# Kernel optimization log

Hardware: AMD Instinct MI355X
Metric: run time of the kernel (lower is better)

The kernel has to match this reference:

```python
import jax, jax.numpy as jnp
import numpy as np

N = 100000      # nodes
E = 1600000     # edges (avg degree 16)
F_IN = 128      # num_features
H = 128         # hidden_channels
OUT = 64        # out_channels


def _glorot(key, shape):
    lim = float(np.sqrt(6.0 / (shape[0] + shape[1])))
    return jax.random.uniform(key, shape, jnp.float32, -lim, lim)


def setup_inputs() -> dict:
    key = jax.random.key(0)
    ks = jax.random.split(key, 5)
    x = jax.random.normal(ks[0], (N, F_IN), jnp.float32)
    edge_index = jax.random.randint(ks[1], (2, E), 0, N, dtype=jnp.int64)
    W1 = _glorot(ks[2], (F_IN, H)); b1 = jnp.zeros((H,), jnp.float32)
    W2 = _glorot(ks[3], (H, H));    b2 = jnp.zeros((H,), jnp.float32)
    W3 = _glorot(ks[4], (H, OUT));  b3 = jnp.zeros((OUT,), jnp.float32)
    return {"x": x, "edge_index": edge_index,
            "W1": W1, "b1": b1, "W2": W2, "b2": b2, "W3": W3, "b3": b3}


def _gcn_conv(h, src, dst, norm, W, b, n):
    # PyG GCNConv: linear transform, then sym-normalized scatter aggregation, then bias
    h = h @ W                                   # [N, d_out]
    msg = h[src] * norm[:, None]                # gather + scale, [E+N, d_out]
    agg = jax.ops.segment_sum(msg, dst, num_segments=n)
    return agg + b


def reference(x, edge_index, W1, b1, W2, b2, W3, b3):
    n = x.shape[0]
    # add self-loops (GCNConv default add_self_loops=True)
    loop = jnp.arange(n, dtype=edge_index.dtype)
    src = jnp.concatenate([edge_index[0], loop])
    dst = jnp.concatenate([edge_index[1], loop])
    # symmetric normalization deg^-1/2[src] * deg^-1/2[dst]
    deg = jax.ops.segment_sum(jnp.ones_like(dst, x.dtype), dst, num_segments=n)
    dinv = jnp.where(deg > 0, jax.lax.rsqrt(deg), 0.0)
    norm = dinv[src] * dinv[dst]

    h = jax.nn.relu(_gcn_conv(x, src, dst, norm, W1, b1, n))  # dropout p=0 -> no-op
    h = jax.nn.relu(_gcn_conv(h, src, dst, norm, W2, b2, n))
    h = _gcn_conv(h, src, dst, norm, W3, b3, n)
    return jax.nn.log_softmax(h, axis=1)
```

## Files before the change

### kernel.cpp

```cpp
#include <hip/hip_runtime.h>
#include <stdint.h>
#include <math.h>

#define FIN 128

typedef __attribute__((ext_vector_type(8))) short short8v;
typedef __attribute__((ext_vector_type(4))) float float4v;
typedef __attribute__((ext_vector_type(2))) float float2v;

__device__ __forceinline__ uint32_t f2_to_bf2(float x, float y) {
    uint32_t r;
    asm("v_cvt_pk_bf16_f32 %0, %1, %2" : "=v"(r) : "v"(x), "v"(y));
    return r;
}
__device__ __forceinline__ unsigned short f_to_bf(float x) {
    union { float f; uint32_t i; } a;
    a.f = x;
    uint32_t u = a.i + 0x7FFF + ((a.i >> 16) & 1);
    return (unsigned short)(u >> 16);
}
__device__ __forceinline__ void acc16_fp8_pk(float2v* acc2, uint4 v) {
    uint32_t us[4] = {v.x, v.y, v.z, v.w};
#pragma unroll
    for (int q = 0; q < 4; ++q) {
        acc2[q * 2 + 0] += __builtin_amdgcn_cvt_pk_f32_fp8(us[q], false);
        acc2[q * 2 + 1] += __builtin_amdgcn_cvt_pk_f32_fp8(us[q], true);
    }
}

template <int CTRL>
__device__ __forceinline__ float dppmov(float x) {
    int i = __builtin_bit_cast(int, x);
    int r = __builtin_amdgcn_update_dpp(i, i, CTRL, 0xF, 0xF, false);
    return __builtin_bit_cast(float, r);
}
__device__ __forceinline__ float swz16f(float x) {
    int r = __builtin_amdgcn_ds_swizzle(__builtin_bit_cast(int, x), 0x401F);
    return __builtin_bit_cast(float, r);
}

__device__ __forceinline__ int edge_at(const void* ei, long long idx, int is32) {
    return is32 ? ((const int*)ei)[idx] : (int)((const long long*)ei)[idx];
}

#define SP_CHUNK 4096
__global__ __launch_bounds__(256) void splitA_kernel(const void* __restrict__ ei,
                                                     int* __restrict__ gCnt,
                                                     uint32_t* __restrict__ buf1,
                                                     int E, int capS) {
    __shared__ int hist[16];
    __shared__ int gbase[16];
    __shared__ int lflag;
    int t = threadIdx.x;
    if (t < 16) hist[t] = 0;
    if (t == 0) lflag = 0;
    long long base = (long long)blockIdx.x * SP_CHUNK;
    __syncthreads();
    {
        long long e = base + t;
        if (e < E && ((const int*)ei)[2 * e + 1] != 0) atomicOr(&lflag, 1);
    }
    __syncthreads();
    int is32 = lflag;
    uint32_t lrec[16], rec[16];
#pragma unroll
    for (int j = 0; j < 16; ++j) {
        long long e = base + t + j * 256;
        if (e < E) {
            int s = edge_at(ei, e, is32);
            int d = edge_at(ei, (long long)E + e, is32);
            int b = d >> 13;
            int lofs = atomicAdd(&hist[b], 1);
            lrec[j] = ((uint32_t)lofs << 4) | (uint32_t)b;
            rec[j] = ((uint32_t)s << 13) | (uint32_t)(d & 8191);
        } else
            lrec[j] = 0xFFFFFFFFu;
    }
    __syncthreads();
    if (t < 16) gbase[t] = atomicAdd(&gCnt[t], hist[t]);
    __syncthreads();
#pragma unroll
    for (int j = 0; j < 16; ++j) {
        if (lrec[j] != 0xFFFFFFFFu) {
            int b = lrec[j] & 15;
            int pos = gbase[b] + (int)(lrec[j] >> 4);
            if (pos < capS) buf1[(size_t)b * capS + pos] = rec[j];
        }
    }
}

__global__ __launch_bounds__(256) void splitB_kernel(const int* __restrict__ gCnt,
                                                     const uint32_t* __restrict__ buf1,
                                                     int* __restrict__ cnt2,
                                                     uint32_t* __restrict__ buf2,
                                                     int capS, int cap2, int NB) {
    __shared__ int hist[128];
    __shared__ int gbase[128];
    int t = threadIdx.x;
    int s = blockIdx.y;
    if (t < 128) hist[t] = 0;
    __syncthreads();
    int m = gCnt[s];
    if (m > capS) m = capS;
    long long base = (long long)blockIdx.x * SP_CHUNK;
    uint32_t lrec[16], r32[16];
#pragma unroll
    for (int j = 0; j < 16; ++j) {
        long long i = base + t + j * 256;
        if (i < m) {
            uint32_t r = buf1[(size_t)s * capS + i];
            int d13 = (int)(r & 8191u);
            int sub = d13 >> 6;
            int lofs = atomicAdd(&hist[sub], 1);
            lrec[j] = ((uint32_t)lofs << 7) | (uint32_t)sub;
            r32[j] = ((r >> 13) << 6) | (uint32_t)(d13 & 63);
        } else
            lrec[j] = 0xFFFFFFFFu;
    }
    __syncthreads();
    if (t < 128) {
        int g = s * 128 + t;
        gbase[t] = (g < NB) ? atomicAdd(&cnt2[g], hist[t]) : 0;
    }
    __syncthreads();
#pragma unroll
    for (int j = 0; j < 16; ++j) {
        if (lrec[j] != 0xFFFFFFFFu) {
            int sub = lrec[j] & 127;
            int pos = gbase[sub] + (int)(lrec[j] >> 7);
            if (pos < cap2) buf2[(size_t)(s * 128 + sub) * cap2 + pos] = r32[j];
        }
    }
}

__global__ __launch_bounds__(256) void binBC_kernel(const int* __restrict__ cnt2,
                                                    const uint32_t* __restrict__ buf2,
                                                    int* __restrict__ cnt,
                                                    float* __restrict__ dinv,
                                                    int* __restrict__ rowstart,
                                                    int* __restrict__ col,
                                                    int n, int cap2) {
    __shared__ int h[64];
    __shared__ int rowst[64];
    __shared__ int cur[64];
    __shared__ int sc[64];
    int bin = blockIdx.x;
    int t = threadIdx.x;
    if (t < 64) {
        h[t] = (bin * 64 + t < n) ? 1 : 0;
        cur[t] = 1;
    }
    __syncthreads();
    int m = cnt2[bin];
    if (m > cap2) m = cap2;
    const uint32_t* buf = buf2 + (size_t)bin * cap2;
    for (int i = t; i < m; i += 256) atomicAdd(&h[buf[i] & 63], 1);
    __syncthreads();
    int c = 0, pc = 0;
    if (t < 64) { c = h[t]; pc = (c + 3) & ~3; sc[t] = pc; }
    __syncthreads();
    for (int off = 1; off < 64; off <<= 1) {
        int v = 0;
        if (t < 64 && t >= off) v = sc[t - off];
        __syncthreads();
        if (t < 64) sc[t] += v;
        __syncthreads();
    }
    if (t < 64) {
        int node = bin * 64 + t;
        int base = bin * cap2;
        int st = base + sc[t] - pc;
        rowst[t] = st;
        if (node < n) {
            cnt[node] = c;
            dinv[node] = rsqrtf((float)c);
            rowstart[node] = st;
            col[st] = node;
            for (int k = c; k < pc; ++k) col[st + k] = n;
        }
    }
    __syncthreads();
    for (int i = t; i < m; i += 256) {
        uint32_t rec = buf[i];
        int d6 = rec & 63;
        int off = atomicAdd(&cur[d6], 1);
        col[rowst[d6] + off] = (int)(rec >> 6);
    }
}

__global__ __launch_bounds__(256) void wconv_all(const float* __restrict__ W1,
                                                 const float* __restrict__ W2,
                                                 const float* __restrict__ W3,
                                                 unsigned short* __restrict__ Wf1,
                                                 unsigned short* __restrict__ Wf2,
                                                 unsigned short* __restrict__ Wf3) {
    int idx = blockIdx.x * 256 + threadIdx.x;
    const float* W;
    unsigned short* Wf;
    int NCOL, base;
    if (idx < 2048)      { W = W1; Wf = Wf1; NCOL = 128; base = idx; }
    else if (idx < 4096) { W = W2; Wf = Wf2; NCOL = 128; base = idx - 2048; }
    else if (idx < 5120) { W = W3; Wf = Wf3; NCOL = 64;  base = idx - 4096; }
    else return;
    int f = base >> 6, l = base & 63;
    int ct = f >> 2, ks = f & 3;
    int nn = ct * 16 + (l & 15);
    int k0 = ks * 32 + (l >> 4) * 8;
    uint32_t pk[4];
#pragma unroll
    for (int j = 0; j < 4; ++j) {
        float a = W[(size_t)(k0 + 2 * j) * NCOL + nn];
        float b = W[(size_t)(k0 + 2 * j + 1) * NCOL + nn];
        pk[j] = f2_to_bf2(a, b);
    }
    uint4 v = make_uint4(pk[0], pk[1], pk[2], pk[3]);
    ((uint4*)Wf)[base] = v;
}

template <int NCOL, int A_FP32, int OUT_FP8>
__global__ __launch_bounds__(256) void gemm_mfma(const void* __restrict__ Av,
                                                 const unsigned short* __restrict__ Wf,
                                                 const float* __restrict__ dinv,
                                                 void* __restrict__ Cv, int n) {
    __shared__ unsigned short lds[NCOL * 128];
    const int t = threadIdx.x;
    if (blockIdx.x == 0 && t < NCOL / 4)
        ((uint32_t*)Cv)[(size_t)n * (NCOL / 4) + t] = 0;
    for (int i = t; i < NCOL * 16; i += 256)
        ((uint4*)lds)[i] = ((const uint4*)Wf)[i];
    __syncthreads();

    const int wave = t >> 6, lane = t & 63;
    const int row0 = blockIdx.x * 64 + wave * 16;
    const int m = lane & 15, quad = lane >> 4;
    int arow = row0 + m;
    if (arow >= n) arow = n - 1;

    short8v a[4];
    if (A_FP32) {
        const float* A = (const float*)Av;
#pragma unroll
        for (int ks = 0; ks < 4; ++ks) {
            float4 lo = *(const float4*)(A + (size_t)arow * 128 + ks * 32 + quad * 8);
            float4 hi = *(const float4*)(A + (size_t)arow * 128 + ks * 32 + quad * 8 + 4);
            union { short8v v; uint32_t u[4]; } pk;
            pk.u[0] = f2_to_bf2(lo.x, lo.y);
            pk.u[1] = f2_to_bf2(lo.z, lo.w);
            pk.u[2] = f2_to_bf2(hi.x, hi.y);
            pk.u[3] = f2_to_bf2(hi.z, hi.w);
            a[ks] = pk.v;
        }
    } else {
        const unsigned short* A = (const unsigned short*)Av;
#pragma unroll
        for (int ks = 0; ks < 4; ++ks)
            a[ks] = *(const short8v*)(A + (size_t)arow * 128 + ks * 32 + quad * 8);
    }

    const int cr0 = row0 + quad * 4;
    float ds[4];
#pragma unroll
    for (int r = 0; r < 4; ++r) {
        int gr = cr0 + r;
        ds[r] = (gr < n) ? dinv[gr] : 0.0f;
    }
#pragma unroll
    for (int ct = 0; ct < NCOL / 16; ++ct) {
        float4v acc = {0.0f, 0.0f, 0.0f, 0.0f};
#pragma unroll
        for (int ks = 0; ks < 4; ++ks) {
            int f = ct * 4 + ks;
            short8v b = *(const short8v*)(lds + ((size_t)(f * 64 + lane)) * 8);
            acc = __builtin_amdgcn_mfma_f32_16x16x32_bf16(a[ks], b, acc, 0, 0, 0);
        }
#pragma unroll
        for (int r = 0; r < 4; ++r) {
            int gr = cr0 + r;
            if (gr < n) {
                float val = acc[r] * ds[r];
                if (OUT_FP8) {
                    int u = __builtin_amdgcn_cvt_pk_fp8_f32(val, val, 0, false);
                    ((unsigned char*)Cv)[(size_t)gr * NCOL + ct * 16 + m] =
                        (unsigned char)(u & 0xFF);
                } else {
                    ((unsigned short*)Cv)[(size_t)gr * NCOL + ct * 16 + m] = f_to_bf(val);
                }
            }
        }
    }
}

__global__ __launch_bounds__(256) void agg_relu_128_fp8(
        const uint32_t* __restrict__ T8, const int* __restrict__ rowstart,
        const int* __restrict__ cnt, const int* __restrict__ col,
        const float* __restrict__ dinv, const float* __restrict__ bias,
        uint32_t* __restrict__ outHb, int n) {
    int wid = blockIdx.x * 4 + (threadIdx.x >> 6);
    int lane = threadIdx.x & 63;
    int slot = lane & 3, j = (lane >> 2) & 7, sel = lane >> 5;
    int nodeA = wid * 2;
    int node = nodeA + sel;
    if (nodeA >= n) return;
    bool valid = node < n;
    int nd = valid ? node : nodeA;
    int start = rowstart[nd];
    int c = cnt[nd];
    int nit = valid ? (((c + 3) & ~3) >> 2) : 0;

    float2v acc2[8];
#pragma unroll
    for (int k = 0; k < 8; ++k) acc2[k] = (float2v){0.0f, 0.0f};
    const uint4* T4 = (const uint4*)T8;
    int bp = start + slot;
    int s0 = col[bp];
    s0 = (0 < nit) ? s0 : n;
    uint4 vN = T4[(size_t)s0 * 8 + j];
    int s1 = col[bp + 4];
    s1 = (1 < nit) ? s1 : n;
    uint4 vM = T4[(size_t)s1 * 8 + j];
    for (int it = 0; it < nit; ++it) {
        int s2 = col[bp + (it + 2) * 4];
        s2 = (it + 2 < nit) ? s2 : n;
        uint4 vP = T4[(size_t)s2 * 8 + j];
        acc16_fp8_pk(acc2, vN);
        vN = vM;
        vM = vP;
    }
    float* acc = (float*)acc2;
#pragma unroll
    for (int k = 0; k < 16; ++k) acc[k] += dppmov<0xB1>(acc[k]);
#pragma unroll
    for (int k = 0; k < 16; ++k) acc[k] += dppmov<0x4E>(acc[k]);
    if (slot == 0 && valid) {
        float di = dinv[node];
        const float4* b4 = (const float4*)bias;
        float r[16];
#pragma unroll
        for (int q = 0; q < 4; ++q) {
            float4 bb = b4[j * 4 + q];
            r[q * 4 + 0] = fmaxf(di * acc[q * 4 + 0] + bb.x, 0.0f);
            r[q * 4 + 1] = fmaxf(di * acc[q * 4 + 1] + bb.y, 0.0f);
            r[q * 4 + 2] = fmaxf(di * acc[q * 4 + 2] + bb.z, 0.0f);
            r[q * 4 + 3] = fmaxf(di * acc[q * 4 + 3] + bb.w, 0.0f);
        }
        uint4 o0, o1;
        o0.x = f2_to_bf2(r[0], r[1]);   o0.y = f2_to_bf2(r[2], r[3]);
        o0.z = f2_to_bf2(r[4], r[5]);   o0.w = f2_to_bf2(r[6], r[7]);
        o1.x = f2_to_bf2(r[8], r[9]);   o1.y = f2_to_bf2(r[10], r[11]);
        o1.z = f2_to_bf2(r[12], r[13]); o1.w = f2_to_bf2(r[14], r[15]);
        *(uint4*)(outHb + (size_t)node * 64 + j * 8) = o0;
        *(uint4*)(outHb + (size_t)node * 64 + j * 8 + 4) = o1;
    }
}

__global__ __launch_bounds__(256) void agg_lsm_64_fp8(
        const uint32_t* __restrict__ T8, const int* __restrict__ rowstart,
        const int* __restrict__ cnt, const int* __restrict__ col,
        const float* __restrict__ dinv, const float* __restrict__ bias,
        float* __restrict__ out, int n) {
    int wid = blockIdx.x * 4 + (threadIdx.x >> 6);
    int lane = threadIdx.x & 63;
    int slot = (lane & 3) + ((lane >> 4) & 1) * 4;
    int j = (lane >> 2) & 3, sel = lane >> 5;
    int nodeA = wid * 2;
    int node = nodeA + sel;
    if (nodeA >= n) return;
    bool valid = node < n;
    int nd = valid ? node : nodeA;
    int start = rowstart[nd];
    int c = cnt[nd];
    int pend = valid ? (start + ((c + 3) & ~3)) : start;
    int nit = valid ? (((c + 3) & ~3) + 7) >> 3 : 0;

    float2v acc2[8];
#pragma unroll
    for (int k = 0; k < 8; ++k) acc2[k] = (float2v){0.0f, 0.0f};
    const uint4* T4 = (const uint4*)T8;
    int bp = start + slot;
    int i0 = bp;
    int s0 = col[i0];
    s0 = (i0 < pend) ? s0 : n;
    uint4 vN = T4[(size_t)s0 * 4 + j];
    int i1 = bp + 8;
    int s1 = col[i1];
    s1 = (i1 < pend) ? s1 : n;
    uint4 vM = T4[(size_t)s1 * 4 + j];
    for (int it = 0; it < nit; ++it) {
        int i2 = bp + (it + 2) * 8;
        int s2 = col[i2];
        s2 = (i2 < pend) ? s2 : n;
        uint4 vP = T4[(size_t)s2 * 4 + j];
        acc16_fp8_pk(acc2, vN);
        vN = vM;
        vM = vP;
    }
    float* acc = (float*)acc2;
#pragma unroll
    for (int k = 0; k < 16; ++k) acc[k] += dppmov<0xB1>(acc[k]);
#pragma unroll
    for (int k = 0; k < 16; ++k) acc[k] += dppmov<0x4E>(acc[k]);
#pragma unroll
    for (int k = 0; k < 16; ++k) acc[k] += swz16f(acc[k]);
    float di = dinv[nd];
    const float4* b4 = (const float4*)bias;
    float r[16];
#pragma unroll
    for (int q = 0; q < 4; ++q) {
        float4 bb = b4[j * 4 + q];
        r[q * 4 + 0] = di * acc[q * 4 + 0] + bb.x;
        r[q * 4 + 1] = di * acc[q * 4 + 1] + bb.y;
        r[q * 4 + 2] = di * acc[q * 4 + 2] + bb.z;
        r[q * 4 + 3] = di * acc[q * 4 + 3] + bb.w;
    }
    float m0 = fmaxf(fmaxf(r[0], r[1]), fmaxf(r[2], r[3]));
    float m1 = fmaxf(fmaxf(r[4], r[5]), fmaxf(r[6], r[7]));
    float m2 = fmaxf(fmaxf(r[8], r[9]), fmaxf(r[10], r[11]));
    float m3 = fmaxf(fmaxf(r[12], r[13]), fmaxf(r[14], r[15]));
    float m = fmaxf(fmaxf(m0, m1), fmaxf(m2, m3));
    m = fmaxf(m, dppmov<0x124>(m));
    m = fmaxf(m, dppmov<0x128>(m));
    float e0 = __expf(r[0] - m) + __expf(r[1] - m) + __expf(r[2] - m) +
               __expf(r[3] - m);
    float e1 = __expf(r[4] - m) + __expf(r[5] - m) + __expf(r[6] - m) +
               __expf(r[7] - m);
    float e2 = __expf(r[8] - m) + __expf(r[9] - m) + __expf(r[10] - m) +
               __expf(r[11] - m);
    float e3 = __expf(r[12] - m) + __expf(r[13] - m) + __expf(r[14] - m) +
               __expf(r[15] - m);
    float ss = (e0 + e1) + (e2 + e3);
    ss += dppmov<0x124>(ss);
    ss += dppmov<0x128>(ss);
    float lg = m + __logf(ss);
    if (slot == 0 && valid) {
#pragma unroll
        for (int q = 0; q < 4; ++q) {
            float4 o = make_float4(r[q * 4 + 0] - lg, r[q * 4 + 1] - lg,
                                   r[q * 4 + 2] - lg, r[q * 4 + 3] - lg);
            *(float4*)(out + (size_t)node * 64 + j * 16 + q * 4) = o;
        }
    }
}

extern "C" void kernel_launch(void* const* d_in, const int* in_sizes, int n_in,
                              void* d_out, int out_size, void* d_ws, size_t ws_size,
                              hipStream_t stream) {
    const float* x  = (const float*)d_in[0];
    const void*  ei = d_in[1];
    const float* W1 = (const float*)d_in[2];
    const float* b1 = (const float*)d_in[3];
    const float* W2 = (const float*)d_in[4];
    const float* b2 = (const float*)d_in[5];
    const float* W3 = (const float*)d_in[6];
    const float* b3 = (const float*)d_in[7];
    float* out = (float*)d_out;

    const int n = in_sizes[0] / FIN;
    const int E = in_sizes[1] / 2;

    char* p = (char*)d_ws;
    auto carve = [&](size_t bytes) {
        char* q = p;
        p += (bytes + 255) & ~(size_t)255;
        return q;
    };
    const int NB = (n + 63) / 64;
    const int NS = (n + 8191) / 8192;

    long long meanS = (long long)E * 8192 / n;
    int capS = (int)(meanS + 8 * (long long)sqrt((double)meanS) + 1024);
    capS = (capS + 15) & ~15;
    long long mean2 = (long long)E * 64 / n;
    int cap2 = (int)(mean2 + 8 * (long long)sqrt((double)mean2) + 832);
    cap2 = (cap2 + 15) & ~15;

    int*   cnt      = (int*)carve((size_t)n * 4);
    int*   rowstart = (int*)carve((size_t)n * 4);
    float* dinv     = (float*)carve((size_t)n * 4);
    int*   colb     = (int*)carve(((size_t)NB * cap2 + 4096) * 4);
    int*   gCnt     = (int*)carve((size_t)(16 + NB) * 4);
    int*   cnt2     = gCnt + 16;
    size_t Tbytes = (size_t)n * 128 + 256;
    size_t Hbytes = (size_t)n * 128 * 2;
    char*  TH = carve(Tbytes + Hbytes);
    void*  T  = (void*)TH;
    unsigned short* Hb = (unsigned short*)(TH + Tbytes);
    unsigned short* Wf1 = (unsigned short*)carve(128 * 128 * 2);
    unsigned short* Wf2 = (unsigned short*)carve(128 * 128 * 2);
    unsigned short* Wf3 = (unsigned short*)carve(128 * 64 * 2);

    size_t buf1B = ((size_t)NS * capS * 4 + 255) & ~(size_t)255;
    uint32_t* buf1 = (uint32_t*)TH;
    uint32_t* buf2 = (uint32_t*)(TH + buf1B);
    size_t avail2 = (Tbytes + Hbytes > buf1B) ? (Tbytes + Hbytes - buf1B) : 0;
    size_t maxc2 = avail2 / ((size_t)NB * 4);
    if ((size_t)cap2 > maxc2) cap2 = (int)maxc2;

    hipMemsetAsync(gCnt, 0, (size_t)(16 + NB) * 4, stream);

    const int gagg2 = ((n + 1) / 2 + 3) / 4;
    const int ggemm = (n + 63) / 64;
    const int gsplitA = (E + SP_CHUNK - 1) / SP_CHUNK;
    const int gsplitBx = (capS + SP_CHUNK - 1) / SP_CHUNK;

    splitA_kernel<<<gsplitA, 256, 0, stream>>>(ei, gCnt, buf1, E, capS);
    splitB_kernel<<<dim3(gsplitBx, NS), 256, 0, stream>>>(gCnt, buf1, cnt2, buf2, capS,
                                                          cap2, NB);
    binBC_kernel<<<NB, 256, 0, stream>>>(cnt2, buf2, cnt, dinv, rowstart, colb, n,
                                         cap2);
    wconv_all<<<20, 256, 0, stream>>>(W1, W2, W3, Wf1, Wf2, Wf3);

    gemm_mfma<128, 1, 1><<<ggemm, 256, 0, stream>>>(x, Wf1, dinv, T, n);
    agg_relu_128_fp8<<<gagg2, 256, 0, stream>>>((const uint32_t*)T, rowstart, cnt,
                                                colb, dinv, b1, (uint32_t*)Hb, n);
    gemm_mfma<128, 0, 1><<<ggemm, 256, 0, stream>>>(Hb, Wf2, dinv, T, n);
    agg_relu_128_fp8<<<gagg2, 256, 0, stream>>>((const uint32_t*)T, rowstart, cnt,
                                                colb, dinv, b2, (uint32_t*)Hb, n);
    gemm_mfma<64, 0, 1><<<ggemm, 256, 0, stream>>>(Hb, Wf3, dinv, T, n);
    agg_lsm_64_fp8<<<gagg2, 256, 0, stream>>>((const uint32_t*)T, rowstart, cnt, colb,
                                              dinv, b3, out, n);
}
```

Measured before the change: 305.8 us.

## Pad CSR rows to 8 and remap lanes so feature chunks are contiguous

Row padding in the CSR build goes from multiples of 4 to multiples of 8, and the bucket capacity grows to make room for the extra padding. In both aggregation kernels the lane mapping is swapped so adjacent lanes read adjacent 16-byte chunks of the same source row, which should coalesce each gather into contiguous row segments. The 128-wide kernel now handles two neighbors per iteration, with a deeper software pipeline. The cross-lane reduction patterns are changed to match the new layout. In exchange, padding adds more dummy loads and a larger column buffer.

```diff
diff --git a/kernel.cpp b/kernel.cpp
--- a/kernel.cpp
+++ b/kernel.cpp
@@ -157,7 +157,7 @@
     for (int i = t; i < m; i += 256) atomicAdd(&h[buf[i] & 63], 1);
     __syncthreads();
     int c = 0, pc = 0;
-    if (t < 64) { c = h[t]; pc = (c + 3) & ~3; sc[t] = pc; }
+    if (t < 64) { c = h[t]; pc = (c + 7) & ~7; sc[t] = pc; }
     __syncthreads();
     for (int off = 1; off < 64; off <<= 1) {
         int v = 0;
@@ -297,7 +297,7 @@
         uint32_t* __restrict__ outHb, int n) {
     int wid = blockIdx.x * 4 + (threadIdx.x >> 6);
     int lane = threadIdx.x & 63;
-    int slot = lane & 3, j = (lane >> 2) & 7, sel = lane >> 5;
+    int j = lane & 7, slot = (lane >> 3) & 3, sel = lane >> 5;
     int nodeA = wid * 2;
     int node = nodeA + sel;
     if (nodeA >= n) return;
@@ -305,32 +305,38 @@
     int nd = valid ? node : nodeA;
     int start = rowstart[nd];
     int c = cnt[nd];
-    int nit = valid ? (((c + 3) & ~3) >> 2) : 0;
+    int nit = valid ? (((c + 7) & ~7) >> 3) : 0;
 
     float2v acc2[8];
 #pragma unroll
     for (int k = 0; k < 8; ++k) acc2[k] = (float2v){0.0f, 0.0f};
     const uint4* T4 = (const uint4*)T8;
     int bp = start + slot;
-    int s0 = col[bp];
-    s0 = (0 < nit) ? s0 : n;
-    uint4 vN = T4[(size_t)s0 * 8 + j];
-    int s1 = col[bp + 4];
-    s1 = (1 < nit) ? s1 : n;
-    uint4 vM = T4[(size_t)s1 * 8 + j];
+    int sA0 = col[bp];          sA0 = (0 < nit) ? sA0 : n;
+    int sA1 = col[bp + 4];      sA1 = (0 < nit) ? sA1 : n;
+    uint4 vA0 = T4[(size_t)sA0 * 8 + j];
+    uint4 vA1 = T4[(size_t)sA1 * 8 + j];
+    int sB0 = col[bp + 8];      sB0 = (1 < nit) ? sB0 : n;
+    int sB1 = col[bp + 12];     sB1 = (1 < nit) ? sB1 : n;
+    uint4 vB0 = T4[(size_t)sB0 * 8 + j];
+    uint4 vB1 = T4[(size_t)sB1 * 8 + j];
     for (int it = 0; it < nit; ++it) {
-        int s2 = col[bp + (it + 2) * 4];
-        s2 = (it + 2 < nit) ? s2 : n;
-        uint4 vP = T4[(size_t)s2 * 8 + j];
-        acc16_fp8_pk(acc2, vN);
-        vN = vM;
-        vM = vP;
+        int sC0 = col[bp + (it + 2) * 8];
+        sC0 = (it + 2 < nit) ? sC0 : n;
+        int sC1 = col[bp + (it + 2) * 8 + 4];
+        sC1 = (it + 2 < nit) ? sC1 : n;
+        uint4 vC0 = T4[(size_t)sC0 * 8 + j];
+        uint4 vC1 = T4[(size_t)sC1 * 8 + j];
+        acc16_fp8_pk(acc2, vA0);
+        acc16_fp8_pk(acc2, vA1);
+        vA0 = vB0; vA1 = vB1;
+        vB0 = vC0; vB1 = vC1;
     }
     float* acc = (float*)acc2;
 #pragma unroll
-    for (int k = 0; k < 16; ++k) acc[k] += dppmov<0xB1>(acc[k]);
-#pragma unroll
-    for (int k = 0; k < 16; ++k) acc[k] += dppmov<0x4E>(acc[k]);
+    for (int k = 0; k < 16; ++k) acc[k] += dppmov<0x128>(acc[k]);
+#pragma unroll
+    for (int k = 0; k < 16; ++k) acc[k] += swz16f(acc[k]);
     if (slot == 0 && valid) {
         float di = dinv[node];
         const float4* b4 = (const float4*)bias;
@@ -360,8 +366,7 @@
         float* __restrict__ out, int n) {
     int wid = blockIdx.x * 4 + (threadIdx.x >> 6);
     int lane = threadIdx.x & 63;
-    int slot = (lane & 3) + ((lane >> 4) & 1) * 4;
-    int j = (lane >> 2) & 3, sel = lane >> 5;
+    int j = lane & 3, slot = (lane >> 2) & 7, sel = lane >> 5;
     int nodeA = wid * 2;
     int node = nodeA + sel;
     if (nodeA >= n) return;
@@ -369,36 +374,30 @@
     int nd = valid ? node : nodeA;
     int start = rowstart[nd];
     int c = cnt[nd];
-    int pend = valid ? (start + ((c + 3) & ~3)) : start;
-    int nit = valid ? (((c + 3) & ~3) + 7) >> 3 : 0;
+    int nit = valid ? (((c + 7) & ~7) >> 3) : 0;
 
     float2v acc2[8];
 #pragma unroll
     for (int k = 0; k < 8; ++k) acc2[k] = (float2v){0.0f, 0.0f};
     const uint4* T4 = (const uint4*)T8;
     int bp = start + slot;
-    int i0 = bp;
-    int s0 = col[i0];
-    s0 = (i0 < pend) ? s0 : n;
-    uint4 vN = T4[(size_t)s0 * 4 + j];
-    int i1 = bp + 8;
-    int s1 = col[i1];
-    s1 = (i1 < pend) ? s1 : n;
-    uint4 vM = T4[(size_t)s1 * 4 + j];
+    int s0 = col[bp];           s0 = (0 < nit) ? s0 : n;
+    uint4 vA = T4[(size_t)s0 * 4 + j];
+    int s1 = col[bp + 8];       s1 = (1 < nit) ? s1 : n;
+    uint4 vB = T4[(size_t)s1 * 4 + j];
     for (int it = 0; it < nit; ++it) {
-        int i2 = bp + (it + 2) * 8;
-        int s2 = col[i2];
-        s2 = (i2 < pend) ? s2 : n;
-        uint4 vP = T4[(size_t)s2 * 4 + j];
-        acc16_fp8_pk(acc2, vN);
-        vN = vM;
-        vM = vP;
+        int s2 = col[bp + (it + 2) * 8];
+        s2 = (it + 2 < nit) ? s2 : n;
+        uint4 vC = T4[(size_t)s2 * 4 + j];
+        acc16_fp8_pk(acc2, vA);
+        vA = vB;
+        vB = vC;
     }
     float* acc = (float*)acc2;
 #pragma unroll
-    for (int k = 0; k < 16; ++k) acc[k] += dppmov<0xB1>(acc[k]);
-#pragma unroll
-    for (int k = 0; k < 16; ++k) acc[k] += dppmov<0x4E>(acc[k]);
+    for (int k = 0; k < 16; ++k) acc[k] += dppmov<0x124>(acc[k]);
+#pragma unroll
+    for (int k = 0; k < 16; ++k) acc[k] += dppmov<0x128>(acc[k]);
 #pragma unroll
     for (int k = 0; k < 16; ++k) acc[k] += swz16f(acc[k]);
     float di = dinv[nd];
@@ -417,8 +416,8 @@
     float m2 = fmaxf(fmaxf(r[8], r[9]), fmaxf(r[10], r[11]));
     float m3 = fmaxf(fmaxf(r[12], r[13]), fmaxf(r[14], r[15]));
     float m = fmaxf(fmaxf(m0, m1), fmaxf(m2, m3));
-    m = fmaxf(m, dppmov<0x124>(m));
-    m = fmaxf(m, dppmov<0x128>(m));
+    m = fmaxf(m, dppmov<0xB1>(m));
+    m = fmaxf(m, dppmov<0x4E>(m));
     float e0 = __expf(r[0] - m) + __expf(r[1] - m) + __expf(r[2] - m) +
                __expf(r[3] - m);
     float e1 = __expf(r[4] - m) + __expf(r[5] - m) + __expf(r[6] - m) +
@@ -428,8 +427,8 @@
     float e3 = __expf(r[12] - m) + __expf(r[13] - m) + __expf(r[14] - m) +
                __expf(r[15] - m);
     float ss = (e0 + e1) + (e2 + e3);
-    ss += dppmov<0x124>(ss);
-    ss += dppmov<0x128>(ss);
+    ss += dppmov<0xB1>(ss);
+    ss += dppmov<0x4E>(ss);
     float lg = m + __logf(ss);
     if (slot == 0 && valid) {
 #pragma unroll
@@ -470,7 +469,7 @@
     int capS = (int)(meanS + 8 * (long long)sqrt((double)meanS) + 1024);
     capS = (capS + 15) & ~15;
     long long mean2 = (long long)E * 64 / n;
-    int cap2 = (int)(mean2 + 8 * (long long)sqrt((double)mean2) + 832);
+    int cap2 = (int)(mean2 + 8 * (long long)sqrt((double)mean2) + 1152);
     cap2 = (cap2 + 15) & ~15;
 
     int*   cnt      = (int*)carve((size_t)n * 4);
```

Result: faster. 292.3 us (-4.4%).
